# Optimization experiments

Measured on AMD Instinct MI355X. Metric: run time of the kernel, lower is better.

## Reference

```python
import jax, jax.numpy as jnp
import numpy as np

SR = 44100        # sample rate (init arg)
WIN = 442         # FFT window length from tensor[i:i+442]
HOP = 4           # loop stride
NBINS = 221       # kept spectrum bins x[:221]
THR = 0.01        # threshold passed to inner fftLayer
REL = 0.0594      # relative pitch-change threshold
BIN_HZ = 100.0    # argmax*100 -> frequency


def _windows_and_mag(tensor):
    n = tensor.shape[0]
    n_win = (n - WIN + HOP - 1) // HOP
    starts = jnp.arange(n_win) * HOP
    windows = tensor[starts[:, None] + jnp.arange(WIN)[None, :]]
    spec = jnp.fft.fft(windows, axis=-1)[:, :NBINS]           # complex64 [n_win, 221]
    spec = jnp.where(jnp.abs(spec) < THR, jnp.zeros_like(spec), spec)  # fftLayer threshold
    mag = jnp.abs(spec.real) + jnp.abs(spec.imag)             # |re| + |im|, as in forward
    return mag, starts


def setup_inputs() -> dict:
    key = jax.random.key(0)
    return {"tensor": jax.random.normal(key, (1_000_000,), dtype=jnp.float32)}


def reference(tensor):
    mag, starts = _windows_and_mag(tensor)
    # per-window dominant frequency: argmax bin * 100 Hz
    tmp = jnp.argmax(mag, axis=-1).astype(jnp.float32) * BIN_HZ    # [n_win]
    i_samp = starts.astype(jnp.float32)                            # sample index of each window

    def step(carry, x):
        maxF, Ftime = carry
        t, i = x
        cond = jnp.abs(maxF - t) > maxF * REL
        emit_f = maxF
        emit_d = (i - Ftime) * 1000.0 / SR
        maxF = jnp.where(cond, t, maxF)
        Ftime = jnp.where(cond, i, Ftime)
        return (maxF, Ftime), (cond, emit_f, emit_d)

    (maxF, Ftime), (flags, freqs, durs) = jax.lax.scan(
        step, (jnp.float32(0.0), jnp.float32(0.0)), (tmp, i_samp))
    # trailing append after the loop: (maxF, (i_last - Ftime)*1000/44100)
    final = jnp.stack([maxF, (i_samp[-1] - Ftime) * 1000.0 / SR])
    # flags marks windows where a note boundary was emitted; (freqs, durs) at those
    # positions are the (maxF, duration_ms) pairs the original appends to `out`.
    return flags, freqs, durs, final
```

## Files before the change

kernel.cpp:

```cpp
#include <hip/hip_runtime.h>

#define WIN 442
#define HOP 4
#define NBINS 221
#define LC 128
#define SPAN 960
#define GSZ 32

constexpr double kPI = 3.14159265358979323846264338327950288;

constexpr double tsin_poly(double r) {
    double t = r, s = r;
    for (int n = 1; n <= 9; ++n) { t *= -(r * r) / ((2.0 * n) * (2.0 * n + 1.0)); s += t; }
    return s;
}
constexpr double tcos_poly(double r) {
    double t = 1.0, c = 1.0;
    for (int n = 1; n <= 9; ++n) { t *= -(r * r) / ((2.0 * n - 1.0) * (2.0 * n)); c += t; }
    return c;
}
struct SC { double s, c; };
constexpr SC tsincos(double a) {
    int q = (int)(a / (kPI / 2) + 0.5);
    double r = a - q * (kPI / 2);
    double sr = tsin_poly(r), cr = tcos_poly(r);
    switch (q & 3) {
        case 0: return {sr, cr};
        case 1: return {cr, -sr};
        case 2: return {-sr, -cr};
        default: return {-cr, sr};
    }
}
struct TabF { float c[WIN]; float s[WIN]; };
constexpr TabF make_tabf() {
    TabF t{};
    for (int i = 0; i < WIN; ++i) {
        SC sc = tsincos(2.0 * kPI * (double)i / 442.0);
        t.c[i] = (float)sc.c; t.s[i] = (float)(-sc.s);
    }
    return t;
}
struct TabR { double c4[NBINS], s4[NBINS], c8[NBINS], s8[NBINS]; };
constexpr TabR make_tabr() {
    TabR t{};
    for (int k = 0; k < NBINS; ++k) {
        SC a = tsincos(2.0 * kPI * (double)((4 * k) % WIN) / 442.0);
        t.c4[k] = a.c; t.s4[k] = a.s;
        SC b = tsincos(2.0 * kPI * (double)((8 * k) % WIN) / 442.0);
        t.c8[k] = b.c; t.s8[k] = b.s;
    }
    return t;
}
__constant__ TabF cTabF = make_tabf();
__constant__ TabR cTabR = make_tabr();

static __device__ __forceinline__ unsigned long long shflx64(unsigned long long v, int off) {
    unsigned int lo = (unsigned int)v, hi = (unsigned int)(v >> 32);
    lo = __shfl_xor(lo, off, 64);
    hi = __shfl_xor(hi, off, 64);
    return ((unsigned long long)hi << 32) | lo;
}

__global__ __launch_bounds__(128) void k_slide(
    const float* __restrict__ x, int n, int n_win, int n_chunks,
    int* __restrict__ a_arr, unsigned short* __restrict__ M0) {
    __shared__ __align__(16) float Xs[SPAN];
    __shared__ __align__(16) float Ds_[LC * 4];
    __shared__ unsigned long long cand[LC][9];

    const int tid = threadIdx.x;
    const int lane = tid & 63;
    const int wc = tid >> 6;
    const int chunk = blockIdx.x;
    const int s0 = chunk * (LC * HOP);

    for (int i = tid; i < SPAN; i += 128) {
        int g = s0 + i;
        Xs[i] = (g < n) ? x[g] : 0.0f;
    }
    __syncthreads();
    for (int r = tid; r < LC * 4; r += 128) Ds_[r] = Xs[r + WIN] - Xs[r];
    __syncthreads();

    const int wlen = min(LC, n_win - chunk * LC);

    const int k0 = lane + 128 * wc, k1 = k0 + 64;
    const bool a0 = (k0 < NBINS), a1 = (k1 < NBINS);
    const int kk0 = a0 ? k0 : 0, kk1 = a1 ? k1 : 0;
    const unsigned int lo0 = 255u - (unsigned)k0, lo1 = 255u - (unsigned)k1;

    float ec0[8], es0[8], ec1[8], es1[8];
    {
        int t0 = 0, t1 = 0;
#pragma unroll
        for (int m = 1; m < 8; ++m) {
            t0 += kk0; if (t0 >= WIN) t0 -= WIN;
            ec0[m] = cTabF.c[t0]; es0[m] = cTabF.s[t0];
            t1 += kk1; if (t1 >= WIN) t1 -= WIN;
            ec1[m] = cTabF.c[t1]; es1[m] = cTabF.s[t1];
        }
    }
    double C40 = a0 ? cTabR.c4[kk0] : 0.0, S40 = a0 ? cTabR.s4[kk0] : 0.0;
    double C41 = a1 ? cTabR.c4[kk1] : 0.0, S41 = a1 ? cTabR.s4[kk1] : 0.0;
    const double C80 = cTabR.c8[kk0], S80 = cTabR.s8[kk0];
    const double C81 = cTabR.c8[kk1], S81 = cTabR.s8[kk1];

    double S0r, S0i, S1r, S1i;
    {
        float xa = Xs[440], xb = Xs[441];
        S0r = (double)fmaf(xb, ec0[1], xa);
        S0i = (double)(xb * es0[1]);
        S1r = (double)fmaf(xb, ec1[1], xa);
        S1i = (double)(xb * es1[1]);
        const float4* Xq = (const float4*)Xs;
#pragma unroll 1
        for (int t = 54; t >= 0; --t) {
            float4 va = Xq[2 * t], vb = Xq[2 * t + 1];
            float Dr0 = va.x;
            Dr0 = fmaf(va.y, ec0[1], Dr0); Dr0 = fmaf(va.z, ec0[2], Dr0);
            Dr0 = fmaf(va.w, ec0[3], Dr0); Dr0 = fmaf(vb.x, ec0[4], Dr0);
            Dr0 = fmaf(vb.y, ec0[5], Dr0); Dr0 = fmaf(vb.z, ec0[6], Dr0);
            Dr0 = fmaf(vb.w, ec0[7], Dr0);
            float Di0 = va.y * es0[1];
            Di0 = fmaf(va.z, es0[2], Di0); Di0 = fmaf(va.w, es0[3], Di0);
            Di0 = fmaf(vb.x, es0[4], Di0); Di0 = fmaf(vb.y, es0[5], Di0);
            Di0 = fmaf(vb.z, es0[6], Di0); Di0 = fmaf(vb.w, es0[7], Di0);
            double nr = fma(S0r, C80, fma(S0i, S80, (double)Dr0));
            double ni = fma(S0i, C80, fma(S0r, -S80, (double)Di0));
            S0r = nr; S0i = ni;
            float Dr1 = va.x;
            Dr1 = fmaf(va.y, ec1[1], Dr1); Dr1 = fmaf(va.z, ec1[2], Dr1);
            Dr1 = fmaf(va.w, ec1[3], Dr1); Dr1 = fmaf(vb.x, ec1[4], Dr1);
            Dr1 = fmaf(vb.y, ec1[5], Dr1); Dr1 = fmaf(vb.z, ec1[6], Dr1);
            Dr1 = fmaf(vb.w, ec1[7], Dr1);
            float Di1 = va.y * es1[1];
            Di1 = fmaf(va.z, es1[2], Di1); Di1 = fmaf(va.w, es1[3], Di1);
            Di1 = fmaf(vb.x, es1[4], Di1); Di1 = fmaf(vb.y, es1[5], Di1);
            Di1 = fmaf(vb.z, es1[6], Di1); Di1 = fmaf(vb.w, es1[7], Di1);
            nr = fma(S1r, C81, fma(S1i, S81, (double)Dr1));
            ni = fma(S1i, C81, fma(S1r, -S81, (double)Di1));
            S1r = nr; S1i = ni;
        }
    }
    if (!a0) { S0r = 0.0; S0i = 0.0; }
    if (!a1) { S1r = 0.0; S1i = 0.0; }

    const float4* Dq = (const float4*)Ds_;
    for (int b = 0; b < 16; ++b) {
        unsigned long long key[8];
#pragma unroll
        for (int u = 0; u < 8; ++u) {
            if (b | u) {
                float4 d = Dq[b * 8 + u - 1];
                float Dr0 = fmaf(d.w, ec0[3], fmaf(d.z, ec0[2], fmaf(d.y, ec0[1], d.x)));
                float Di0 = fmaf(d.w, es0[3], fmaf(d.z, es0[2], d.y * es0[1]));
                double nr = S0r + (double)Dr0;
                double ni = S0i + (double)Di0;
                S0r = fma(nr, C40, -(ni * S40));
                S0i = fma(nr, S40, ni * C40);
                float Dr1 = fmaf(d.w, ec1[3], fmaf(d.z, ec1[2], fmaf(d.y, ec1[1], d.x)));
                float Di1 = fmaf(d.w, es1[3], fmaf(d.z, es1[2], d.y * es1[1]));
                nr = S1r + (double)Dr1;
                ni = S1i + (double)Di1;
                S1r = fma(nr, C41, -(ni * S41));
                S1i = fma(nr, S41, ni * C41);
            }
            float m0 = (float)(fabs(S0r) + fabs(S0i));
            float m1 = (float)(fabs(S1r) + fabs(S1i));
            unsigned long long key0 = ((unsigned long long)__float_as_uint(m0) << 32) | lo0;
            unsigned long long key1 = ((unsigned long long)__float_as_uint(m1) << 32) | lo1;
            key[u] = (key1 > key0) ? key1 : key0;
        }
#pragma unroll
        for (int s = 0; s < 4; ++s) {
            const int off = 32 >> s;
#pragma unroll
            for (int u = 0; u < 8; ++u) {
                unsigned long long o = shflx64(key[u], off);
                if (o > key[u]) key[u] = o;
            }
        }
        if (lane < 4) {
#pragma unroll
            for (int u = 0; u < 8; ++u) cand[b * 8 + u][wc * 4 + lane] = key[u];
        }
    }
    __syncthreads();
    int* ti = (int*)Ds_;
    float* tfl = Ds_ + LC;
    if (tid < wlen) {
        unsigned long long best = cand[tid][0];
#pragma unroll
        for (int i = 1; i < 8; ++i) {
            unsigned long long c = cand[tid][i];
            if (c > best) best = c;
        }
        int a = 255 - (int)(best & 255u);
        a_arr[chunk * LC + tid] = a;
        ti[tid] = a;
        tfl[tid] = 100.0f * (float)a;
    }
    __syncthreads();
    for (int b = tid; b < NBINS; b += 128) {
        float mF = 100.0f * (float)b;
        int bin = b, rel = -1;
        for (int i = 0; i < wlen; ++i) {
            float t = tfl[i];
            if (fabsf(mF - t) > mF * 0.0594f) { mF = t; bin = ti[i]; rel = i; }
        }
        M0[chunk * NBINS + b] = (unsigned short)(((rel + 1) << 8) | bin);
    }
}

__global__ __launch_bounds__(256) void k_sm1(const unsigned short* __restrict__ M0,
                                             int n_chunks, int* __restrict__ M1) {
    __shared__ unsigned short sm[GSZ * NBINS];
    int g = blockIdx.x;
    int c0 = g * GSZ;
    int cn = min(GSZ, n_chunks - c0);
    for (int i = threadIdx.x; i < cn * NBINS; i += 256) sm[i] = M0[c0 * NBINS + i];
    __syncthreads();
    int b = threadIdx.x;
    if (b < NBINS) {
        int bin = b, rw = -1;
        for (int i = 0; i < cn; ++i) {
            unsigned short mp = sm[i * NBINS + bin];
            if (mp >> 8) { rw = (c0 + i) * LC + (int)(mp >> 8) - 1; bin = mp & 255; }
        }
        M1[g * NBINS + b] = ((rw + 1) << 8) | bin;
    }
}

__global__ __launch_bounds__(256) void k_e0(const unsigned short* __restrict__ M0,
                                            const int* __restrict__ M1,
                                            int n_chunks, int ngrp,
                                            int* __restrict__ E0) {
    extern __shared__ char dyn[];
    int* m1s = (int*)dyn;
    unsigned short* m0s = (unsigned short*)(m1s + ngrp * NBINS);
    int g = blockIdx.x;
    int c0 = g * GSZ;
    int cn = min(GSZ, n_chunks - c0);
    for (int i = threadIdx.x; i < ngrp * NBINS; i += 256) m1s[i] = M1[i];
    for (int i = threadIdx.x; i < cn * NBINS; i += 256) m0s[i] = M0[c0 * NBINS + i];
    __syncthreads();
    int j = threadIdx.x;
    if (j < cn) {
        int bin = 0, rw = -1;
        for (int i = 0; i < g; ++i) {
            int mp = m1s[i * NBINS + bin];
            if (mp >> 8) { rw = (mp >> 8) - 1; bin = mp & 255; }
        }
        for (int q = 0; q < j; ++q) {
            unsigned short mp = m0s[q * NBINS + bin];
            if (mp >> 8) { rw = (c0 + q) * LC + (int)(mp >> 8) - 1; bin = mp & 255; }
        }
        E0[c0 + j] = ((rw + 1) << 8) | bin;
    }
}

__global__ __launch_bounds__(128) void k_emit(const int* __restrict__ a_arr,
    const int* __restrict__ E0, int n_win,
    float* __restrict__ flags, float* __restrict__ freqs, float* __restrict__ durs,
    float* __restrict__ out_final) {
    __shared__ float tf[LC];
    int j = blockIdx.x;
    int wbeg = j * LC;
    int cnt = n_win - wbeg; if (cnt > LC) cnt = LC;
    if (cnt <= 0) return;
    for (int i = threadIdx.x; i < cnt; i += 128) tf[i] = 100.0f * (float)a_arr[wbeg + i];
    __syncthreads();
    int t = threadIdx.x;
    if (t < cnt) {
        int st = E0[j];
        float maxF = 100.0f * (float)(st & 255);
        int rw = (st >> 8) - 1;
        float Ftime = (rw < 0) ? 0.0f : 4.0f * (float)rw;
        for (int i = 0; i < t; ++i) {
            float tv = tf[i];
            if (fabsf(maxF - tv) > maxF * 0.0594f) {
                maxF = tv; Ftime = 4.0f * (float)(wbeg + i);
            }
        }
        int w = wbeg + t;
        float tv = tf[t];
        float iw = 4.0f * (float)w;
        bool cond = fabsf(maxF - tv) > maxF * 0.0594f;
        flags[w] = cond ? 1.0f : 0.0f;
        freqs[w] = maxF;
        durs[w] = (iw - Ftime) * 1000.0f / 44100.0f;
        if (w == n_win - 1) {
            float fMax = cond ? tv : maxF;
            float fT   = cond ? iw : Ftime;
            out_final[0] = fMax;
            out_final[1] = (iw - fT) * 1000.0f / 44100.0f;
        }
    }
}

extern "C" void kernel_launch(void* const* d_in, const int* in_sizes, int n_in,
                              void* d_out, int out_size, void* d_ws, size_t ws_size,
                              hipStream_t stream) {
    const float* x = (const float*)d_in[0];
    int n = in_sizes[0];
    int n_win = (n - WIN + HOP - 1) / HOP;
    float* out = (float*)d_out;
    char* ws = (char*)d_ws;

    int n_chunks = (n_win + LC - 1) / LC;
    int ngrp = (n_chunks + GSZ - 1) / GSZ;

    int* a_arr         = (int*)(ws + 0);
    unsigned short* M0 = (unsigned short*)(ws + 1000448);
    int* M1            = (int*)(ws + 1864192);
    int* E0            = (int*)(ws + 1919232);

    size_t e0_lds = (size_t)ngrp * NBINS * 4 + (size_t)GSZ * NBINS * 2;

    k_slide<<<dim3(n_chunks), dim3(128), 0, stream>>>(x, n, n_win, n_chunks, a_arr, M0);
    k_sm1<<<dim3(ngrp), dim3(256), 0, stream>>>(M0, n_chunks, M1);
    k_e0<<<dim3(ngrp), dim3(256), e0_lds, stream>>>(M0, M1, n_chunks, ngrp, E0);
    k_emit<<<dim3(n_chunks), dim3(128), 0, stream>>>(a_arr, E0, n_win,
                                                     out, out + (size_t)n_win,
                                                     out + 2 * (size_t)n_win,
                                                     out + 3 * (size_t)n_win);
}
```

Baseline: 167.7 us.

## Fuse group-composition into k_slide via last-block atomic and fold e0 into emit

Removes the k_sm1 and k_e0 launches. The last block of each group, detected with an atomic counter, composes that group's M1 map inside k_slide. Each k_emit block now computes its own starting state serially in thread 0 from global M1/M0, and the bin-map loop handles two bins per thread while deriving the bin from mF. This cuts kernel launches and the intermediate E0 buffer. In exchange it adds a memset, threadfence/atomic overhead, and a serial global-memory chain walk in every emit block.

```diff
diff --git a/kernel.cpp b/kernel.cpp
--- a/kernel.cpp
+++ b/kernel.cpp
@@ -63,10 +63,14 @@
 
 __global__ __launch_bounds__(128) void k_slide(
     const float* __restrict__ x, int n, int n_win, int n_chunks,
-    int* __restrict__ a_arr, unsigned short* __restrict__ M0) {
-    __shared__ __align__(16) float Xs[SPAN];
-    __shared__ __align__(16) float Ds_[LC * 4];
-    __shared__ unsigned long long cand[LC][9];
+    int* __restrict__ a_arr, unsigned short* __restrict__ M0,
+    int* __restrict__ M1, int* __restrict__ cnt) {
+    __shared__ __align__(16) unsigned char smem[15360];
+    __shared__ int composeFlag;
+    float* Xs  = reinterpret_cast<float*>(smem);
+    float* Ds_ = reinterpret_cast<float*>(smem + SPAN * 4);
+    unsigned long long* cand =
+        reinterpret_cast<unsigned long long*>(smem + SPAN * 4 + LC * 16);
 
     const int tid = threadIdx.x;
     const int lane = tid & 63;
@@ -182,100 +186,101 @@
         }
         if (lane < 4) {
 #pragma unroll
-            for (int u = 0; u < 8; ++u) cand[b * 8 + u][wc * 4 + lane] = key[u];
-        }
-    }
-    __syncthreads();
-    int* ti = (int*)Ds_;
-    float* tfl = Ds_ + LC;
+            for (int u = 0; u < 8; ++u) cand[(b * 8 + u) * 9 + wc * 4 + lane] = key[u];
+        }
+    }
+    __syncthreads();
+    float* tfl = Ds_;
     if (tid < wlen) {
-        unsigned long long best = cand[tid][0];
+        unsigned long long best = cand[tid * 9];
 #pragma unroll
         for (int i = 1; i < 8; ++i) {
-            unsigned long long c = cand[tid][i];
+            unsigned long long c = cand[tid * 9 + i];
             if (c > best) best = c;
         }
         int a = 255 - (int)(best & 255u);
         a_arr[chunk * LC + tid] = a;
-        ti[tid] = a;
         tfl[tid] = 100.0f * (float)a;
     }
     __syncthreads();
-    for (int b = tid; b < NBINS; b += 128) {
-        float mF = 100.0f * (float)b;
-        int bin = b, rel = -1;
+    {
+        int b0 = tid, b1 = tid + 128;
+        bool act1 = (b1 < NBINS);
+        float mF0 = 100.0f * (float)b0;
+        float mF1 = act1 ? 100.0f * (float)b1 : 100.0f;
+        int rel0 = -1, rel1 = -1;
         for (int i = 0; i < wlen; ++i) {
             float t = tfl[i];
-            if (fabsf(mF - t) > mF * 0.0594f) { mF = t; bin = ti[i]; rel = i; }
-        }
-        M0[chunk * NBINS + b] = (unsigned short)(((rel + 1) << 8) | bin);
-    }
-}
-
-__global__ __launch_bounds__(256) void k_sm1(const unsigned short* __restrict__ M0,
-                                             int n_chunks, int* __restrict__ M1) {
-    __shared__ unsigned short sm[GSZ * NBINS];
-    int g = blockIdx.x;
-    int c0 = g * GSZ;
-    int cn = min(GSZ, n_chunks - c0);
-    for (int i = threadIdx.x; i < cn * NBINS; i += 256) sm[i] = M0[c0 * NBINS + i];
-    __syncthreads();
-    int b = threadIdx.x;
-    if (b < NBINS) {
-        int bin = b, rw = -1;
+            if (fabsf(mF0 - t) > mF0 * 0.0594f) { mF0 = t; rel0 = i; }
+            if (fabsf(mF1 - t) > mF1 * 0.0594f) { mF1 = t; rel1 = i; }
+        }
+        int bin0 = __float2int_rn(mF0 * 0.01f);
+        M0[chunk * NBINS + b0] = (unsigned short)(((rel0 + 1) << 8) | bin0);
+        if (act1) {
+            int bin1 = __float2int_rn(mF1 * 0.01f);
+            M0[chunk * NBINS + b1] = (unsigned short)(((rel1 + 1) << 8) | bin1);
+        }
+    }
+    __syncthreads();
+    const int grp = chunk / GSZ;
+    const int c0 = grp * GSZ;
+    const int cn = min(GSZ, n_chunks - c0);
+    if (tid == 0) {
+        __threadfence();
+        int old = atomicAdd(&cnt[grp], 1);
+        composeFlag = (old == cn - 1);
+    }
+    __syncthreads();
+    if (composeFlag) {
+        __threadfence();
+        unsigned short* smap = reinterpret_cast<unsigned short*>(smem);
+        for (int i = tid; i < cn * NBINS; i += 128) smap[i] = M0[c0 * NBINS + i];
+        __syncthreads();
+        int b0 = tid, b1 = tid + 128;
+        bool act1 = (b1 < NBINS);
+        int bin0 = b0, bin1 = act1 ? b1 : 0;
+        int rw0 = -1, rw1 = -1;
         for (int i = 0; i < cn; ++i) {
-            unsigned short mp = sm[i * NBINS + bin];
-            if (mp >> 8) { rw = (c0 + i) * LC + (int)(mp >> 8) - 1; bin = mp & 255; }
-        }
-        M1[g * NBINS + b] = ((rw + 1) << 8) | bin;
-    }
-}
-
-__global__ __launch_bounds__(256) void k_e0(const unsigned short* __restrict__ M0,
-                                            const int* __restrict__ M1,
-                                            int n_chunks, int ngrp,
-                                            int* __restrict__ E0) {
-    extern __shared__ char dyn[];
-    int* m1s = (int*)dyn;
-    unsigned short* m0s = (unsigned short*)(m1s + ngrp * NBINS);
-    int g = blockIdx.x;
-    int c0 = g * GSZ;
-    int cn = min(GSZ, n_chunks - c0);
-    for (int i = threadIdx.x; i < ngrp * NBINS; i += 256) m1s[i] = M1[i];
-    for (int i = threadIdx.x; i < cn * NBINS; i += 256) m0s[i] = M0[c0 * NBINS + i];
-    __syncthreads();
-    int j = threadIdx.x;
-    if (j < cn) {
-        int bin = 0, rw = -1;
-        for (int i = 0; i < g; ++i) {
-            int mp = m1s[i * NBINS + bin];
-            if (mp >> 8) { rw = (mp >> 8) - 1; bin = mp & 255; }
-        }
-        for (int q = 0; q < j; ++q) {
-            unsigned short mp = m0s[q * NBINS + bin];
-            if (mp >> 8) { rw = (c0 + q) * LC + (int)(mp >> 8) - 1; bin = mp & 255; }
-        }
-        E0[c0 + j] = ((rw + 1) << 8) | bin;
+            unsigned short mp0 = smap[i * NBINS + bin0];
+            if (mp0 >> 8) { rw0 = (c0 + i) * LC + (int)(mp0 >> 8) - 1; bin0 = mp0 & 255; }
+            unsigned short mp1 = smap[i * NBINS + bin1];
+            if (mp1 >> 8) { rw1 = (c0 + i) * LC + (int)(mp1 >> 8) - 1; bin1 = mp1 & 255; }
+        }
+        M1[grp * NBINS + b0] = ((rw0 + 1) << 8) | bin0;
+        if (act1) M1[grp * NBINS + b1] = ((rw1 + 1) << 8) | bin1;
     }
 }
 
 __global__ __launch_bounds__(128) void k_emit(const int* __restrict__ a_arr,
-    const int* __restrict__ E0, int n_win,
+    const unsigned short* __restrict__ M0, const int* __restrict__ M1, int n_win,
     float* __restrict__ flags, float* __restrict__ freqs, float* __restrict__ durs,
     float* __restrict__ out_final) {
     __shared__ float tf[LC];
+    __shared__ float sh[2];
     int j = blockIdx.x;
     int wbeg = j * LC;
     int cnt = n_win - wbeg; if (cnt > LC) cnt = LC;
     if (cnt <= 0) return;
     for (int i = threadIdx.x; i < cnt; i += 128) tf[i] = 100.0f * (float)a_arr[wbeg + i];
+    if (threadIdx.x == 0) {
+        int g = j / GSZ;
+        int bin = 0, rw = -1;
+        for (int i = 0; i < g; ++i) {
+            int mp = M1[i * NBINS + bin];
+            if (mp >> 8) { rw = (mp >> 8) - 1; bin = mp & 255; }
+        }
+        for (int q = g * GSZ; q < j; ++q) {
+            unsigned short mp = M0[q * NBINS + bin];
+            if (mp >> 8) { rw = q * LC + (int)(mp >> 8) - 1; bin = mp & 255; }
+        }
+        sh[0] = 100.0f * (float)bin;
+        sh[1] = (rw < 0) ? 0.0f : 4.0f * (float)rw;
+    }
     __syncthreads();
     int t = threadIdx.x;
     if (t < cnt) {
-        int st = E0[j];
-        float maxF = 100.0f * (float)(st & 255);
-        int rw = (st >> 8) - 1;
-        float Ftime = (rw < 0) ? 0.0f : 4.0f * (float)rw;
+        float maxF = sh[0];
+        float Ftime = sh[1];
         for (int i = 0; i < t; ++i) {
             float tv = tf[i];
             if (fabsf(maxF - tv) > maxF * 0.0594f) {
@@ -313,14 +318,12 @@
     int* a_arr         = (int*)(ws + 0);
     unsigned short* M0 = (unsigned short*)(ws + 1000448);
     int* M1            = (int*)(ws + 1864192);
-    int* E0            = (int*)(ws + 1919232);
-
-    size_t e0_lds = (size_t)ngrp * NBINS * 4 + (size_t)GSZ * NBINS * 2;
-
-    k_slide<<<dim3(n_chunks), dim3(128), 0, stream>>>(x, n, n_win, n_chunks, a_arr, M0);
-    k_sm1<<<dim3(ngrp), dim3(256), 0, stream>>>(M0, n_chunks, M1);
-    k_e0<<<dim3(ngrp), dim3(256), e0_lds, stream>>>(M0, M1, n_chunks, ngrp, E0);
-    k_emit<<<dim3(n_chunks), dim3(128), 0, stream>>>(a_arr, E0, n_win,
+    int* cnt           = (int*)(ws + 1919232);
+
+    hipMemsetAsync(cnt, 0, (size_t)ngrp * 4, stream);
+    k_slide<<<dim3(n_chunks), dim3(128), 0, stream>>>(x, n, n_win, n_chunks,
+                                                      a_arr, M0, M1, cnt);
+    k_emit<<<dim3(n_chunks), dim3(128), 0, stream>>>(a_arr, M0, M1, n_win,
                                                      out, out + (size_t)n_win,
                                                      out + 2 * (size_t)n_win,
                                                      out + 3 * (size_t)n_win);
```

After: 190.5 us. 1.14x slower.
